# Performance work log

Measured on AMD Instinct MI355X. Metric: run time of the kernel, lower is better.

The kernel has to match this reference:

```python
import jax, jax.numpy as jnp
import numpy as np

QB = 127.0  # 2**(8-1) - 1


def ternary_dequant(w):
    # absmean ternary quantization, then dequantize by scale
    scale = jnp.mean(jnp.abs(w))
    w_t = jnp.clip(jnp.round(w / (scale + 1e-8)), -1.0, 1.0)
    w_t = jnp.where(scale == 0.0, jnp.zeros_like(w), w_t)
    return w_t * scale


def activation_quantize(x):
    # per-row (last-dim) absmax int8 fake-quant
    scale = jnp.max(jnp.abs(x), axis=-1, keepdims=True) / QB
    scale = jnp.maximum(scale, 1e-8)
    return jnp.clip(jnp.round(x / scale), -QB, QB) * scale


def setup_inputs() -> dict:
    key = jax.random.key(0)
    kx, kw = jax.random.split(key)
    x = jax.random.normal(kx, (2, 4096, 4096), dtype=jnp.float32)
    # kaiming_uniform-ish init scale; exact init distribution is irrelevant to the math
    bound = 1.0 / np.sqrt(4096)
    weight = jax.random.uniform(kw, (4096, 4096), dtype=jnp.float32,
                                minval=-bound, maxval=bound)
    return {"x": x, "weight": weight}


def reference(x, weight):
    w_q = ternary_dequant(weight)        # [out, in]
    x_q = activation_quantize(x)         # [b, s, in]
    return jnp.einsum('bsi,oi->bso', x_q, w_q)
```

## Files before the change

kernel.cpp:

```cpp
#include <hip/hip_runtime.h>
#include <stdint.h>
#include <stddef.h>


#define K_DIM 4096
#define M_DIM 8192
#define N_DIM 4096

typedef int v4i __attribute__((ext_vector_type(4)));

__device__ __forceinline__ void async_copy16(void* lds, const void* g) {
  __builtin_amdgcn_global_load_lds(
      (const __attribute__((address_space(1))) unsigned int*)g,
      (__attribute__((address_space(3))) unsigned int*)lds,
      16, 0, 0);
}

__global__ void k_wsum(const float* __restrict__ w, double* __restrict__ partials) {
  const float4* w4 = (const float4*)w;
  int tid = blockIdx.x * 256 + threadIdx.x;
  double s = 0.0;
  for (int i = tid; i < 4194304; i += 262144) {
    float4 v = w4[i];
    s += (double)fabsf(v.x) + (double)fabsf(v.y) +
         (double)fabsf(v.z) + (double)fabsf(v.w);
  }
  for (int off = 32; off > 0; off >>= 1) s += __shfl_down(s, off);
  __shared__ double lsum[4];
  int lane = threadIdx.x & 63, wid = threadIdx.x >> 6;
  if (lane == 0) lsum[wid] = s;
  __syncthreads();
  if (threadIdx.x == 0)
    partials[blockIdx.x] = lsum[0] + lsum[1] + lsum[2] + lsum[3];
}

__global__ void k_quant(const float* __restrict__ w, const double* __restrict__ partials,
                        float* __restrict__ wscale, char* __restrict__ qw,
                        const float* __restrict__ x, char* __restrict__ qx,
                        float* __restrict__ sx) {
  __shared__ float sT;
  __shared__ float lm[4];
  __shared__ float bscale;

  if (blockIdx.x < 2048) {
    if (threadIdx.x < 64) {
      double s = 0.0;
      for (int i = threadIdx.x; i < 1024; i += 64) s += partials[i];
      for (int off = 32; off > 0; off >>= 1) s += __shfl_down(s, off);
      if (threadIdx.x == 0) {
        float sc = (float)(s / 16777216.0);
        if (blockIdx.x == 0) *wscale = sc;
        float d = sc + 1e-8f;
        unsigned lo = 1u, hi = __float_as_uint(d);
        while (hi - lo > 1u) {
          unsigned mid = lo + ((hi - lo) >> 1);
          if (__uint_as_float(mid) / d > 0.5f) hi = mid; else lo = mid;
        }
        sT = __uint_as_float(hi);
      }
    }
    __syncthreads();
    const float T = sT;
    const float4* w4 = (const float4*)w;
    int* q4 = (int*)qw;
    int tid = blockIdx.x * 256 + threadIdx.x;
    for (int i = tid; i < 4194304; i += 524288) {
      float4 v = w4[i];
      int a = (int)(v.x >= T) - (int)(v.x <= -T);
      int b = (int)(v.y >= T) - (int)(v.y <= -T);
      int c = (int)(v.z >= T) - (int)(v.z <= -T);
      int e = (int)(v.w >= T) - (int)(v.w <= -T);
      q4[i] = (a & 255) | ((b & 255) << 8) | ((c & 255) << 16) | ((e & 255) << 24);
    }
  } else {
    int row = blockIdx.x - 2048;
    const float4* xr = (const float4*)(x + (size_t)row * K_DIM);
    float4 v[4];
    float m = 0.f;
#pragma unroll
    for (int c = 0; c < 4; c++) {
      v[c] = xr[threadIdx.x + c * 256];
      m = fmaxf(m, fmaxf(fmaxf(fabsf(v[c].x), fabsf(v[c].y)),
                         fmaxf(fabsf(v[c].z), fabsf(v[c].w))));
    }
    for (int off = 32; off > 0; off >>= 1) m = fmaxf(m, __shfl_down(m, off));
    int lane = threadIdx.x & 63, wid = threadIdx.x >> 6;
    if (lane == 0) lm[wid] = m;
    __syncthreads();
    if (threadIdx.x == 0) {
      float mm = fmaxf(fmaxf(lm[0], lm[1]), fmaxf(lm[2], lm[3]));
      float sc = fmaxf(mm / 127.0f, 1e-8f);
      bscale = sc;
      sx[row] = sc;
    }
    __syncthreads();
    float sc = bscale;
    int* q4 = (int*)(qx + (size_t)row * K_DIM);
#pragma unroll
    for (int c = 0; c < 4; c++) {
      int a = (int)fmaxf(fminf(rintf(v[c].x / sc), 127.f), -127.f);
      int b = (int)fmaxf(fminf(rintf(v[c].y / sc), 127.f), -127.f);
      int cc = (int)fmaxf(fminf(rintf(v[c].z / sc), 127.f), -127.f);
      int e = (int)fmaxf(fminf(rintf(v[c].w / sc), 127.f), -127.f);
      q4[threadIdx.x + c * 256] = (a & 255) | ((b & 255) << 8) | ((cc & 255) << 16) | ((e & 255) << 24);
    }
  }
}

__global__ __launch_bounds__(512, 2) void k_gemm(const char* __restrict__ qx,
                       const char* __restrict__ qw,
                       const float* __restrict__ sx,
                       const float* __restrict__ wscale,
                       float* __restrict__ out) {
  __shared__ char lds[4][32768];

  const int tid = threadIdx.x;
  const int lane = tid & 63;
  const int wave = tid >> 6;
  const int wr = wave >> 2;
  const int wc = wave & 3;

  const int wg = (blockIdx.x & 7) * 64 + (blockIdx.x >> 3);
  const int bm = wg >> 4;
  const int bn = wg & 15;
  const int rowBase = bm * 256;
  const int colBase = bn * 256;

  const int rl = tid >> 2;
  const int kswz = (((tid & 3) ^ ((rl >> 1) & 3)) << 4);
  const char* gA0 = qx + (size_t)(rowBase + rl) * K_DIM + kswz;
  const char* gA1 = gA0 + (size_t)128 * K_DIM;
  const char* gB0 = qw + (size_t)(colBase + rl) * K_DIM + kswz;
  const char* gB1 = gB0 + (size_t)128 * K_DIM;
  const int dOff = wave << 10;

  const int sR = ((lane & 15) >> 1) & 3;
  const int kro = (((lane >> 4) ^ sR) << 4);
  const int aOff = ((wr << 7) + (lane & 15)) * 64 + kro;
  const int bOff = 16384 + ((wc << 6) + (lane & 15)) * 64 + kro;

  v4i acc[8][4] = {};

  auto STAGE = [&](int t) {
    char* b = &lds[t & 3][0];
    const size_t ko = (size_t)t << 6;
    async_copy16(b + dOff,         gA0 + ko);
    async_copy16(b + 8192 + dOff,  gA1 + ko);
    async_copy16(b + 16384 + dOff, gB0 + ko);
    async_copy16(b + 24576 + dOff, gB1 + ko);
  };

  auto PHASES = [&](int t, bool doStage) {
    const char* b_ = &lds[t & 3][0];
    char* sb_ = &lds[(t + 3) & 3][0];
    const size_t ko_ = (size_t)(t + 3) << 6;
    v4i bf[4], a0[4];
#pragma unroll
    for (int n = 0; n < 4; ++n)
      bf[n] = *(const v4i*)(b_ + bOff + n * 1024);
#pragma unroll
    for (int j = 0; j < 4; ++j)
      a0[j] = *(const v4i*)(b_ + aOff + j * 1024);
    if (doStage) {
      async_copy16(sb_ + dOff,        gA0 + ko_);
      async_copy16(sb_ + 8192 + dOff, gA1 + ko_);
    }
    asm volatile("" ::: "memory");
    __builtin_amdgcn_s_barrier();
    __builtin_amdgcn_s_setprio(1);
#pragma unroll
    for (int m = 0; m < 4; ++m)
#pragma unroll
      for (int n = 0; n < 4; ++n)
        acc[m][n] = __builtin_amdgcn_mfma_i32_16x16x64_i8(a0[m], bf[n], acc[m][n], 0, 0, 0);
    __builtin_amdgcn_s_setprio(0);
    asm volatile("" ::: "memory");
    __builtin_amdgcn_s_barrier();
    v4i a1[4];
#pragma unroll
    for (int j = 0; j < 4; ++j)
      a1[j] = *(const v4i*)(b_ + aOff + (4 + j) * 1024);
    if (doStage) {
      async_copy16(sb_ + 16384 + dOff, gB0 + ko_);
      async_copy16(sb_ + 24576 + dOff, gB1 + ko_);
    }
    asm volatile("" ::: "memory");
    __builtin_amdgcn_s_barrier();
    __builtin_amdgcn_s_setprio(1);
#pragma unroll
    for (int m = 0; m < 4; ++m)
#pragma unroll
      for (int n = 0; n < 4; ++n)
        acc[4 + m][n] = __builtin_amdgcn_mfma_i32_16x16x64_i8(a1[m], bf[n], acc[4 + m][n], 0, 0, 0);
    __builtin_amdgcn_s_setprio(0);
  };

  STAGE(0); STAGE(1); STAGE(2);

  for (int t = 0; t < 61; ++t) {
    asm volatile("s_waitcnt vmcnt(8)" ::: "memory");
    __builtin_amdgcn_s_barrier();
    asm volatile("" ::: "memory");
    PHASES(t, true);
  }
  asm volatile("s_waitcnt vmcnt(8)" ::: "memory");
  __builtin_amdgcn_s_barrier();
  asm volatile("" ::: "memory");
  PHASES(61, false);
  asm volatile("s_waitcnt vmcnt(4)" ::: "memory");
  __builtin_amdgcn_s_barrier();
  asm volatile("" ::: "memory");
  PHASES(62, false);
  asm volatile("s_waitcnt vmcnt(0)" ::: "memory");
  __builtin_amdgcn_s_barrier();
  asm volatile("" ::: "memory");
  PHASES(63, false);

  const float swv = *wscale;
  const int col0 = colBase + (wc << 6) + (lane & 15);
  const int row0 = rowBase + (wr << 7) + ((lane >> 4) << 2);
#pragma unroll
  for (int m = 0; m < 8; ++m) {
#pragma unroll
    for (int r = 0; r < 4; ++r) {
      const int row = row0 + m * 16 + r;
      const float s = sx[row] * swv;
#pragma unroll
      for (int n = 0; n < 4; ++n)
        out[(size_t)row * N_DIM + col0 + n * 16] = (float)acc[m][n][r] * s;
    }
  }
}

extern "C" void kernel_launch(void* const* d_in, const int* in_sizes, int n_in,
                              void* d_out, int out_size, void* d_ws, size_t ws_size,
                              hipStream_t stream) {
  const float* x = (const float*)d_in[0];
  const float* w = (const float*)d_in[1];
  float* out = (float*)d_out;
  char* ws = (char*)d_ws;

  double* partials = (double*)ws;
  float* wscale    = (float*)(ws + 8192);
  float* sx        = (float*)(ws + 8448);
  char*  qw        = ws + 41472;
  char*  qx        = ws + 41472 + 16777216;

  k_wsum <<<1024, 256, 0, stream>>>(w, partials);
  k_quant<<<2048 + 8192, 256, 0, stream>>>(w, partials, wscale, qw, x, qx, sx);
  k_gemm <<<32 * 16, 512, 0, stream>>>(qx, qw, sx, wscale, out);
}
```

Baseline: 402.4 us.

## Switch GEMM to double-buffered LDS pipeline with higher occupancy bound

Reduces the int8 GEMM LDS ring from four stages to two and replaces the split two-phase body, which interleaved async loads between MFMA halves, with a single body that loads all fragments, runs 32 MFMAs, then stages the tile two steps ahead. Launch bounds are raised to request four blocks per CU, aiming for more resident waves to hide latency. This shortens prefetch depth and tightens the register budget, which risks spilling the 128-register accumulator and exposing global-load latency.

Measured after the change: 1.388 ms. +244.9%, slower.

```diff
diff --git a/kernel.cpp b/kernel.cpp
--- a/kernel.cpp
+++ b/kernel.cpp
@@ -107,12 +107,12 @@
   }
 }
 
-__global__ __launch_bounds__(512, 2) void k_gemm(const char* __restrict__ qx,
+__global__ __launch_bounds__(512, 4) void k_gemm(const char* __restrict__ qx,
                        const char* __restrict__ qw,
                        const float* __restrict__ sx,
                        const float* __restrict__ wscale,
                        float* __restrict__ out) {
-  __shared__ char lds[4][32768];
+  __shared__ char lds[2][32768];
 
   const int tid = threadIdx.x;
   const int lane = tid & 63;
@@ -142,7 +142,7 @@
   v4i acc[8][4] = {};
 
   auto STAGE = [&](int t) {
-    char* b = &lds[t & 3][0];
+    char* b = &lds[t & 1][0];
     const size_t ko = (size_t)t << 6;
     async_copy16(b + dOff,         gA0 + ko);
     async_copy16(b + 8192 + dOff,  gA1 + ko);
@@ -150,71 +150,39 @@
     async_copy16(b + 24576 + dOff, gB1 + ko);
   };
 
-  auto PHASES = [&](int t, bool doStage) {
-    const char* b_ = &lds[t & 3][0];
-    char* sb_ = &lds[(t + 3) & 3][0];
-    const size_t ko_ = (size_t)(t + 3) << 6;
-    v4i bf[4], a0[4];
+  auto BODY = [&](int t) {
+    const char* b_ = &lds[t & 1][0];
+    v4i bf[4], af[8];
 #pragma unroll
     for (int n = 0; n < 4; ++n)
       bf[n] = *(const v4i*)(b_ + bOff + n * 1024);
 #pragma unroll
-    for (int j = 0; j < 4; ++j)
-      a0[j] = *(const v4i*)(b_ + aOff + j * 1024);
-    if (doStage) {
-      async_copy16(sb_ + dOff,        gA0 + ko_);
-      async_copy16(sb_ + 8192 + dOff, gA1 + ko_);
-    }
+    for (int m = 0; m < 8; ++m)
+      af[m] = *(const v4i*)(b_ + aOff + m * 1024);
     asm volatile("" ::: "memory");
-    __builtin_amdgcn_s_barrier();
     __builtin_amdgcn_s_setprio(1);
 #pragma unroll
-    for (int m = 0; m < 4; ++m)
+    for (int m = 0; m < 8; ++m)
 #pragma unroll
       for (int n = 0; n < 4; ++n)
-        acc[m][n] = __builtin_amdgcn_mfma_i32_16x16x64_i8(a0[m], bf[n], acc[m][n], 0, 0, 0);
-    __builtin_amdgcn_s_setprio(0);
-    asm volatile("" ::: "memory");
-    __builtin_amdgcn_s_barrier();
-    v4i a1[4];
-#pragma unroll
-    for (int j = 0; j < 4; ++j)
-      a1[j] = *(const v4i*)(b_ + aOff + (4 + j) * 1024);
-    if (doStage) {
-      async_copy16(sb_ + 16384 + dOff, gB0 + ko_);
-      async_copy16(sb_ + 24576 + dOff, gB1 + ko_);
-    }
-    asm volatile("" ::: "memory");
-    __builtin_amdgcn_s_barrier();
-    __builtin_amdgcn_s_setprio(1);
-#pragma unroll
-    for (int m = 0; m < 4; ++m)
-#pragma unroll
-      for (int n = 0; n < 4; ++n)
-        acc[4 + m][n] = __builtin_amdgcn_mfma_i32_16x16x64_i8(a1[m], bf[n], acc[4 + m][n], 0, 0, 0);
+        acc[m][n] = __builtin_amdgcn_mfma_i32_16x16x64_i8(af[m], bf[n], acc[m][n], 0, 0, 0);
     __builtin_amdgcn_s_setprio(0);
   };
 
-  STAGE(0); STAGE(1); STAGE(2);
-
-  for (int t = 0; t < 61; ++t) {
-    asm volatile("s_waitcnt vmcnt(8)" ::: "memory");
+  STAGE(0); STAGE(1);
+
+  for (int t = 0; t < 64; ++t) {
+    if (t < 63) asm volatile("s_waitcnt vmcnt(4)" ::: "memory");
+    else        asm volatile("s_waitcnt vmcnt(0)" ::: "memory");
     __builtin_amdgcn_s_barrier();
     asm volatile("" ::: "memory");
-    PHASES(t, true);
-  }
-  asm volatile("s_waitcnt vmcnt(8)" ::: "memory");
-  __builtin_amdgcn_s_barrier();
-  asm volatile("" ::: "memory");
-  PHASES(61, false);
-  asm volatile("s_waitcnt vmcnt(4)" ::: "memory");
-  __builtin_amdgcn_s_barrier();
-  asm volatile("" ::: "memory");
-  PHASES(62, false);
-  asm volatile("s_waitcnt vmcnt(0)" ::: "memory");
-  __builtin_amdgcn_s_barrier();
-  asm volatile("" ::: "memory");
-  PHASES(63, false);
+    BODY(t);
+    if (t < 62) {
+      asm volatile("" ::: "memory");
+      __builtin_amdgcn_s_barrier();
+      STAGE(t + 2);
+    }
+  }
 
   const float swv = *wscale;
   const int col0 = colBase + (wc << 6) + (lane & 15);
```
